# Kernel optimization log

Measured on AMD Instinct MI355X. Metric: run time of the kernel, lower is better.

Reference implementation:

```python
import jax, jax.numpy as jnp
import numpy as np

N_IN = 1000000   # non-empty input octants at depth d
N_OUT = 125000   # parent octants at depth d-1 (stride-2 downsample)
C_IN = 96
C_OUT = 192
K = 8            # 2x2x2 kernel -> 8 children per parent
BN_EPS = 1e-5


def setup_inputs() -> dict:
    key = jax.random.key(0)
    k1, k2, k3, k4 = jax.random.split(key, 4)
    data = jax.random.normal(k1, (N_IN, C_IN), dtype=jnp.float32)
    # child-neighbor table: index into input rows; <0 would mean empty child
    neigh = jax.random.randint(k2, (N_OUT, K), 0, N_IN, dtype=jnp.int64)
    # OctreeConv weights [K, Cin, Cout] + bias, BatchNorm affine params
    fan_in = K * C_IN
    weights = jax.random.normal(k3, (K, C_IN, C_OUT), dtype=jnp.float32) / np.sqrt(fan_in)
    bias = jax.random.normal(k4, (C_OUT,), dtype=jnp.float32) * 0.01
    gamma = jnp.ones((C_OUT,), dtype=jnp.float32)
    beta = jnp.zeros((C_OUT,), dtype=jnp.float32)
    return {"data": data, "weights": weights, "bias": bias,
            "gamma": gamma, "beta": beta, "neigh": neigh}


def reference(data, weights, bias, gamma, beta, neigh):
    # --- OctreeConv, kernel 2x2x2, stride 2, nempty=True ---
    valid = neigh >= 0                                   # [M, K]
    idx = jnp.clip(neigh, 0)                             # safe gather index
    gathered = data[idx]                                 # [M, K, Cin]
    gathered = jnp.where(valid[:, :, None], gathered, 0.0)
    out = jnp.einsum('mkc,kcd->md', gathered, weights) + bias  # [M, Cout]
    # --- BatchNorm1d over node dim (training-mode batch stats) ---
    mean = jnp.mean(out, axis=0)
    var = jnp.var(out, axis=0)                           # biased variance
    out = (out - mean) * jax.lax.rsqrt(var + BN_EPS) * gamma + beta
    return out
```

## Files before the change

### kernel.cpp

```cpp
#include <hip/hip_runtime.h>

#define M_OUT   125000
#define CIN     96
#define COUT    192
#define KOCT    8
#define MT      128
#define LDA     104
#define LDB     104
#define BN_EPS  1e-5f

#define WS_SCALE_OFF 384
#define WS_WT_BYTE   4096

typedef __attribute__((ext_vector_type(8))) short bf16x8;
typedef __attribute__((ext_vector_type(4))) float f32x4;

__device__ __forceinline__ unsigned short f2bf(float f) {
    unsigned int u = __float_as_uint(f);
    u += 0x7FFF + ((u >> 16) & 1);
    return (unsigned short)(u >> 16);
}

__device__ __forceinline__ unsigned int pack2(float a, float b) {
    unsigned int ua = __float_as_uint(a);
    unsigned int ub = __float_as_uint(b);
    ua += 0x7FFF + ((ua >> 16) & 1);
    ub += 0x7FFF + ((ub >> 16) & 1);
    return (ua >> 16) | (ub & 0xFFFF0000u);
}

__global__ void prep_kernel(const float* __restrict__ W, float* __restrict__ ws_f,
                            unsigned short* __restrict__ wt) {
    int gid = blockIdx.x * blockDim.x + threadIdx.x;
    if (gid < 384) ws_f[gid] = 0.0f;
    if (gid < KOCT * COUT * LDA) {
        int c = gid % LDA;
        int rest = gid / LDA;
        int n = rest % COUT;
        int k = rest / COUT;
        float v = (c < CIN) ? W[(k * CIN + c) * COUT + n] : 0.0f;
        wt[gid] = f2bf(v);
    }
}

__global__ __launch_bounds__(256, 2)
void conv_kernel(const float* __restrict__ data,
                 const int* __restrict__ neigh,
                 const float* __restrict__ bias,
                 const unsigned short* __restrict__ wt,
                 float* __restrict__ out,
                 float* __restrict__ gsum) {
    __shared__ unsigned short As[MT * LDA];
    __shared__ unsigned short Bs[COUT * LDB];
    __shared__ int   idxs[MT * KOCT];
    __shared__ float stats[2 * COUT];

    const int t    = threadIdx.x;
    const int wave = t >> 6;
    const int lane = t & 63;
    const int quad = lane >> 4;
    const int l15  = lane & 15;
    const int wr   = wave >> 1;
    const int wc   = wave & 1;
    const int m0   = blockIdx.x * MT;

    {
        int r  = t >> 1;
        int gm = m0 + r;
        int4 v;
        if (gm < M_OUT) {
            v = *reinterpret_cast<const int4*>(neigh + gm * 8 + (t & 1) * 4);
        } else {
            v.x = v.y = v.z = v.w = -1;
        }
        *reinterpret_cast<int4*>(idxs + t * 4) = v;
        for (int i = t; i < 2 * COUT; i += 256) stats[i] = 0.0f;
    }

    const f32x4 vzero = {0.f, 0.f, 0.f, 0.f};
    f32x4 acc[4][6];
#pragma unroll
    for (int i = 0; i < 4; ++i)
#pragma unroll
        for (int j = 0; j < 6; ++j) acc[i][j] = vzero;

    __syncthreads();

    for (int k = 0; k < KOCT; ++k) {
#pragma unroll
        for (int j = 0; j < 12; ++j) {
            int lin = j * 256 + t;
            int row = lin / 24;
            int f4  = lin - row * 24;
            int idx = idxs[row * 8 + k];
            unsigned int lo = 0u, hi = 0u;
            if (idx >= 0) {
                float4 v = *reinterpret_cast<const float4*>(data + (size_t)idx * CIN + f4 * 4);
                lo = pack2(v.x, v.y);
                hi = pack2(v.z, v.w);
            }
            uint2 p; p.x = lo; p.y = hi;
            *reinterpret_cast<uint2*>(&As[row * LDA + f4 * 4]) = p;
        }
        {
            const uint4* src = reinterpret_cast<const uint4*>(wt + k * COUT * LDB);
            uint4* dst = reinterpret_cast<uint4*>(Bs);
#pragma unroll
            for (int j = 0; j < 10; ++j) {
                int i = j * 256 + t;
                if (i < (COUT * LDB * 2) / 16) dst[i] = src[i];
            }
        }
        __syncthreads();

#pragma unroll
        for (int ks = 0; ks < 3; ++ks) {
            bf16x8 af[4], bfr[6];
#pragma unroll
            for (int rt = 0; rt < 4; ++rt) {
                int row = wr * 64 + rt * 16 + l15;
                af[rt] = *reinterpret_cast<const bf16x8*>(&As[row * LDA + ks * 32 + quad * 8]);
            }
#pragma unroll
            for (int ct = 0; ct < 6; ++ct) {
                int n = wc * 96 + ct * 16 + l15;
                bfr[ct] = *reinterpret_cast<const bf16x8*>(&Bs[n * LDB + ks * 32 + quad * 8]);
            }
#pragma unroll
            for (int rt = 0; rt < 4; ++rt)
#pragma unroll
                for (int ct = 0; ct < 6; ++ct)
                    acc[rt][ct] = __builtin_amdgcn_mfma_f32_16x16x32_bf16(
                        af[rt], bfr[ct], acc[rt][ct], 0, 0, 0);
        }
        __syncthreads();
    }

#pragma unroll
    for (int ct = 0; ct < 6; ++ct) {
        int col = wc * 96 + ct * 16 + l15;
        float b = bias[col];
        float s1 = 0.f, s2 = 0.f;
#pragma unroll
        for (int rt = 0; rt < 4; ++rt) {
#pragma unroll
            for (int r = 0; r < 4; ++r) {
                int gm = m0 + wr * 64 + rt * 16 + quad * 4 + r;
                if (gm < M_OUT) {
                    float v = acc[rt][ct][r] + b;
                    out[(size_t)gm * COUT + col] = v;
                    s1 += v;
                    s2 += v * v;
                }
            }
        }
        atomicAdd(&stats[col], s1);
        atomicAdd(&stats[COUT + col], s2);
    }
    __syncthreads();
    for (int i = t; i < COUT; i += 256) {
        atomicAdd(&gsum[i], stats[i]);
        atomicAdd(&gsum[COUT + i], stats[COUT + i]);
    }
}

__global__ void finalize_kernel(const float* __restrict__ gsum,
                                const float* __restrict__ gamma,
                                const float* __restrict__ beta,
                                float* __restrict__ ss) {
    int c = threadIdx.x;
    if (c < COUT) {
        float inv_m = 1.0f / (float)M_OUT;
        float mean = gsum[c] * inv_m;
        float var  = gsum[COUT + c] * inv_m - mean * mean;
        float rstd = rsqrtf(var + BN_EPS);
        float sc   = gamma[c] * rstd;
        ss[c]        = sc;
        ss[COUT + c] = beta[c] - mean * sc;
    }
}

__global__ void norm_kernel(float* __restrict__ out, const float* __restrict__ ss) {
    __shared__ float s_scale[COUT], s_shift[COUT];
    for (int i = threadIdx.x; i < COUT; i += blockDim.x) {
        s_scale[i] = ss[i];
        s_shift[i] = ss[COUT + i];
    }
    __syncthreads();
    const int total4 = M_OUT * COUT / 4;
    int stride = gridDim.x * blockDim.x;
    for (int i = blockIdx.x * blockDim.x + threadIdx.x; i < total4; i += stride) {
        float4 v = reinterpret_cast<float4*>(out)[i];
        int c4 = (i % (COUT / 4)) * 4;
        v.x = v.x * s_scale[c4 + 0] + s_shift[c4 + 0];
        v.y = v.y * s_scale[c4 + 1] + s_shift[c4 + 1];
        v.z = v.z * s_scale[c4 + 2] + s_shift[c4 + 2];
        v.w = v.w * s_scale[c4 + 3] + s_shift[c4 + 3];
        reinterpret_cast<float4*>(out)[i] = v;
    }
}

extern "C" void kernel_launch(void* const* d_in, const int* in_sizes, int n_in,
                              void* d_out, int out_size, void* d_ws, size_t ws_size,
                              hipStream_t stream) {
    const float* data  = (const float*)d_in[0];
    const float* W     = (const float*)d_in[1];
    const float* bias  = (const float*)d_in[2];
    const float* gamma = (const float*)d_in[3];
    const float* beta  = (const float*)d_in[4];
    const int*   neigh = (const int*)d_in[5];
    float* out  = (float*)d_out;
    float* ws_f = (float*)d_ws;
    unsigned short* wt = (unsigned short*)((char*)d_ws + WS_WT_BYTE);

    prep_kernel<<<(KOCT * COUT * LDA + 255) / 256, 256, 0, stream>>>(W, ws_f, wt);

    int grid1 = (M_OUT + MT - 1) / MT;
    conv_kernel<<<grid1, 256, 0, stream>>>(data, neigh, bias, wt, out, ws_f);

    finalize_kernel<<<1, 192, 0, stream>>>(ws_f, gamma, beta, ws_f + WS_SCALE_OFF);

    norm_kernel<<<4096, 256, 0, stream>>>(out, ws_f + WS_SCALE_OFF);
}
```

Measured before the change: 659.3 us.

## Double-buffer gathered A tile, read weights from global, shrink tile to 64 rows

The conv kernel halves the row tile to 64 and loads each wave's weight fragments straight from global (L2-resident) memory instead of staging them in LDS. The gathered input rows go into a double-buffered LDS tile, so the gather for the next child octant overlaps the MFMA work on the current one, with one barrier per step. Neighbor indices sit in registers, and the batch-norm stats are reduced with wave shuffles and written with direct global atomics instead of an LDS stage. In exchange, each block re-reads the weights from global memory for half as many rows, there are more blocks, and global atomic traffic grows.

```diff
diff --git a/kernel.cpp b/kernel.cpp
--- a/kernel.cpp
+++ b/kernel.cpp
@@ -4,9 +4,8 @@
 #define CIN     96
 #define COUT    192
 #define KOCT    8
-#define MT      128
+#define MT      64
 #define LDA     104
-#define LDB     104
 #define BN_EPS  1e-5f
 
 #define WS_SCALE_OFF 384
@@ -43,109 +42,116 @@
     }
 }
 
-__global__ __launch_bounds__(256, 2)
+__global__ __launch_bounds__(256, 3)
 void conv_kernel(const float* __restrict__ data,
                  const int* __restrict__ neigh,
                  const float* __restrict__ bias,
                  const unsigned short* __restrict__ wt,
                  float* __restrict__ out,
                  float* __restrict__ gsum) {
-    __shared__ unsigned short As[MT * LDA];
-    __shared__ unsigned short Bs[COUT * LDB];
-    __shared__ int   idxs[MT * KOCT];
-    __shared__ float stats[2 * COUT];
+    __shared__ alignas(16) unsigned short As[2][MT * LDA];
 
     const int t    = threadIdx.x;
-    const int wave = t >> 6;
     const int lane = t & 63;
+    const int w    = t >> 6;
     const int quad = lane >> 4;
     const int l15  = lane & 15;
-    const int wr   = wave >> 1;
-    const int wc   = wave & 1;
+    const int grow = t >> 2;
+    const int qt   = t & 3;
     const int m0   = blockIdx.x * MT;
 
+    int idx8[8];
     {
-        int r  = t >> 1;
-        int gm = m0 + r;
-        int4 v;
+        int gm = m0 + grow;
         if (gm < M_OUT) {
-            v = *reinterpret_cast<const int4*>(neigh + gm * 8 + (t & 1) * 4);
+            int4 a = *reinterpret_cast<const int4*>(neigh + (size_t)gm * 8);
+            int4 b = *reinterpret_cast<const int4*>(neigh + (size_t)gm * 8 + 4);
+            idx8[0] = a.x; idx8[1] = a.y; idx8[2] = a.z; idx8[3] = a.w;
+            idx8[4] = b.x; idx8[5] = b.y; idx8[6] = b.z; idx8[7] = b.w;
         } else {
-            v.x = v.y = v.z = v.w = -1;
-        }
-        *reinterpret_cast<int4*>(idxs + t * 4) = v;
-        for (int i = t; i < 2 * COUT; i += 256) stats[i] = 0.0f;
+#pragma unroll
+            for (int i = 0; i < 8; ++i) idx8[i] = -1;
+        }
     }
 
     const f32x4 vzero = {0.f, 0.f, 0.f, 0.f};
-    f32x4 acc[4][6];
+    const float4 fzero = {0.f, 0.f, 0.f, 0.f};
+    f32x4 acc[4][3];
 #pragma unroll
     for (int i = 0; i < 4; ++i)
 #pragma unroll
-        for (int j = 0; j < 6; ++j) acc[i][j] = vzero;
-
+        for (int j = 0; j < 3; ++j) acc[i][j] = vzero;
+
+    {
+        int idx = idx8[0];
+        const float4* src = reinterpret_cast<const float4*>(
+                                data + (size_t)(idx < 0 ? 0 : idx) * CIN) + qt;
+#pragma unroll
+        for (int i = 0; i < 6; ++i) {
+            float4 g = (idx >= 0) ? src[i * 4] : fzero;
+            uint2 p; p.x = pack2(g.x, g.y); p.y = pack2(g.z, g.w);
+            *reinterpret_cast<uint2*>(&As[0][grow * LDA + (qt + 4 * i) * 4]) = p;
+        }
+    }
     __syncthreads();
 
     for (int k = 0; k < KOCT; ++k) {
-#pragma unroll
-        for (int j = 0; j < 12; ++j) {
-            int lin = j * 256 + t;
-            int row = lin / 24;
-            int f4  = lin - row * 24;
-            int idx = idxs[row * 8 + k];
-            unsigned int lo = 0u, hi = 0u;
-            if (idx >= 0) {
-                float4 v = *reinterpret_cast<const float4*>(data + (size_t)idx * CIN + f4 * 4);
-                lo = pack2(v.x, v.y);
-                hi = pack2(v.z, v.w);
+        const int buf = k & 1;
+
+        bf16x8 bfr[3][3];
+#pragma unroll
+        for (int ks = 0; ks < 3; ++ks)
+#pragma unroll
+            for (int ct = 0; ct < 3; ++ct) {
+                int col = w * 48 + ct * 16 + l15;
+                bfr[ks][ct] = *reinterpret_cast<const bf16x8*>(
+                    wt + ((size_t)k * COUT + col) * LDA + ks * 32 + quad * 8);
             }
-            uint2 p; p.x = lo; p.y = hi;
-            *reinterpret_cast<uint2*>(&As[row * LDA + f4 * 4]) = p;
-        }
+
+        float4 g[6];
+        int idxn = (k < KOCT - 1) ? idx8[k + 1] : -1;
         {
-            const uint4* src = reinterpret_cast<const uint4*>(wt + k * COUT * LDB);
-            uint4* dst = reinterpret_cast<uint4*>(Bs);
-#pragma unroll
-            for (int j = 0; j < 10; ++j) {
-                int i = j * 256 + t;
-                if (i < (COUT * LDB * 2) / 16) dst[i] = src[i];
+            const float4* srcn = reinterpret_cast<const float4*>(
+                                     data + (size_t)(idxn < 0 ? 0 : idxn) * CIN) + qt;
+#pragma unroll
+            for (int i = 0; i < 6; ++i) g[i] = (idxn >= 0) ? srcn[i * 4] : fzero;
+        }
+
+#pragma unroll
+        for (int ks = 0; ks < 3; ++ks) {
+            bf16x8 af[4];
+#pragma unroll
+            for (int rt = 0; rt < 4; ++rt)
+                af[rt] = *reinterpret_cast<const bf16x8*>(
+                    &As[buf][(rt * 16 + l15) * LDA + ks * 32 + quad * 8]);
+#pragma unroll
+            for (int rt = 0; rt < 4; ++rt)
+#pragma unroll
+                for (int ct = 0; ct < 3; ++ct)
+                    acc[rt][ct] = __builtin_amdgcn_mfma_f32_16x16x32_bf16(
+                        af[rt], bfr[ks][ct], acc[rt][ct], 0, 0, 0);
+        }
+
+        if (k < KOCT - 1) {
+#pragma unroll
+            for (int i = 0; i < 6; ++i) {
+                uint2 p; p.x = pack2(g[i].x, g[i].y); p.y = pack2(g[i].z, g[i].w);
+                *reinterpret_cast<uint2*>(&As[buf ^ 1][grow * LDA + (qt + 4 * i) * 4]) = p;
             }
         }
         __syncthreads();
-
-#pragma unroll
-        for (int ks = 0; ks < 3; ++ks) {
-            bf16x8 af[4], bfr[6];
-#pragma unroll
-            for (int rt = 0; rt < 4; ++rt) {
-                int row = wr * 64 + rt * 16 + l15;
-                af[rt] = *reinterpret_cast<const bf16x8*>(&As[row * LDA + ks * 32 + quad * 8]);
-            }
-#pragma unroll
-            for (int ct = 0; ct < 6; ++ct) {
-                int n = wc * 96 + ct * 16 + l15;
-                bfr[ct] = *reinterpret_cast<const bf16x8*>(&Bs[n * LDB + ks * 32 + quad * 8]);
-            }
-#pragma unroll
-            for (int rt = 0; rt < 4; ++rt)
-#pragma unroll
-                for (int ct = 0; ct < 6; ++ct)
-                    acc[rt][ct] = __builtin_amdgcn_mfma_f32_16x16x32_bf16(
-                        af[rt], bfr[ct], acc[rt][ct], 0, 0, 0);
-        }
-        __syncthreads();
-    }
-
-#pragma unroll
-    for (int ct = 0; ct < 6; ++ct) {
-        int col = wc * 96 + ct * 16 + l15;
+    }
+
+#pragma unroll
+    for (int ct = 0; ct < 3; ++ct) {
+        int col = w * 48 + ct * 16 + l15;
         float b = bias[col];
         float s1 = 0.f, s2 = 0.f;
 #pragma unroll
         for (int rt = 0; rt < 4; ++rt) {
 #pragma unroll
             for (int r = 0; r < 4; ++r) {
-                int gm = m0 + wr * 64 + rt * 16 + quad * 4 + r;
+                int gm = m0 + rt * 16 + quad * 4 + r;
                 if (gm < M_OUT) {
                     float v = acc[rt][ct][r] + b;
                     out[(size_t)gm * COUT + col] = v;
@@ -154,13 +160,12 @@
                 }
             }
         }
-        atomicAdd(&stats[col], s1);
-        atomicAdd(&stats[COUT + col], s2);
-    }
-    __syncthreads();
-    for (int i = t; i < COUT; i += 256) {
-        atomicAdd(&gsum[i], stats[i]);
-        atomicAdd(&gsum[COUT + i], stats[COUT + i]);
+        s1 += __shfl_xor(s1, 16); s1 += __shfl_xor(s1, 32);
+        s2 += __shfl_xor(s2, 16); s2 += __shfl_xor(s2, 32);
+        if (quad == 0) {
+            atomicAdd(&gsum[col], s1);
+            atomicAdd(&gsum[COUT + col], s2);
+        }
     }
 }
 
```

After: 713.6 us. +8.2%, slower.
